# Performance work log

Measured on AMD Instinct MI355X. Metric: run time of the kernel, lower is better.

Reference implementation:

```python
import jax, jax.numpy as jnp
import numpy as np

HEADS = 8
DIM_HEAD = 32
DIM = 256
HIDDEN = HEADS * DIM_HEAD  # 256


def setup_inputs() -> dict:
    key = jax.random.key(0)
    ks = jax.random.split(key, 6)
    B, T, C, H, W = 4, 16, DIM, 32, 32
    x = jax.random.normal(ks[0], (B, T, C, H, W), dtype=jnp.float32)
    rel_pos = jax.random.normal(ks[1], (HEADS, T, T), dtype=jnp.float32)
    # 1x1 conv weights == channel-mixing matrices
    w_qkv = jax.random.normal(ks[2], (3 * HIDDEN, C), dtype=jnp.float32) * (C ** -0.5)
    b_qkv = jnp.zeros((3 * HIDDEN,), dtype=jnp.float32)
    w_out = jax.random.normal(ks[3], (C, HIDDEN), dtype=jnp.float32) * (HIDDEN ** -0.5)
    b_out = jnp.zeros((C,), dtype=jnp.float32)
    return {"x": x, "rel_pos": rel_pos, "w_qkv": w_qkv, "b_qkv": b_qkv,
            "w_out": w_out, "b_out": b_out}


def reference(x, rel_pos, w_qkv, b_qkv, w_out, b_out):
    B, T, C, H, W = x.shape
    scale = DIM_HEAD ** -0.5
    # 1x1 conv QKV projection: (B,T,C,H,W) x (3*hidden, C) -> (B,T,H,W,3*hidden)
    qkv = jnp.einsum('btchw,oc->bthwo', x, w_qkv) + b_qkv
    q, k, v = jnp.split(qkv, 3, axis=-1)
    # split heads: (B,T,H,W,heads,dim_head); attention over T per (b,h,w,head)
    q = q.reshape(B, T, H, W, HEADS, DIM_HEAD) * scale
    k = k.reshape(B, T, H, W, HEADS, DIM_HEAD)
    v = v.reshape(B, T, H, W, HEADS, DIM_HEAD)
    # sim: (B,H,W,heads,T,T)
    sim = jnp.einsum('bihwnd,bjhwnd->bhwnij', q, k)
    sim = sim + rel_pos  # (heads,T,T) broadcasts over (B,H,W)
    attn = jax.nn.softmax(sim, axis=-1)
    out = jnp.einsum('bhwnij,bjhwnd->bihwnd', attn, v)  # (B,T,H,W,heads,dh)
    out = out.reshape(B, T, H, W, HIDDEN)
    # 1x1 conv output projection back to C channels
    y = jnp.einsum('bthwe,ce->bthwc', out, w_out) + b_out
    return jnp.transpose(y, (0, 1, 4, 2, 3))  # (B,T,C,H,W)
```

## Files before the change

### kernel.cpp

```cpp
#include <hip/hip_runtime.h>
#include <hip/hip_bf16.h>

typedef __attribute__((ext_vector_type(8))) short bf16x8;
typedef __attribute__((ext_vector_type(4))) float f32x4;
typedef __attribute__((ext_vector_type(16))) float f32x16;

namespace {

constexpr int kT = 16;
constexpr int kC = 256;
constexpr int kHW = 1024;

__device__ __forceinline__ unsigned short f2bf(float f) {
  unsigned int x;
  __builtin_memcpy(&x, &f, 4);
  x += 0x7fff + ((x >> 16) & 1);
  return (unsigned short)(x >> 16);
}
__device__ __forceinline__ unsigned int pack2(float a, float b) {
  return (unsigned int)f2bf(a) | ((unsigned int)f2bf(b) << 16);
}

__global__ __launch_bounds__(256) void prep(const float* __restrict__ x,
                                            const float* __restrict__ wqkv,
                                            const float* __restrict__ wout,
                                            unsigned short* __restrict__ xT,
                                            unsigned short* __restrict__ wAll) {
  __shared__ unsigned short ts[64 * 72];
  const int bx = blockIdx.x;
  const int tid = threadIdx.x;
  if (bx < 4096) {
    const int cc = bx & 3, hc = (bx >> 2) & 15, t = (bx >> 6) & 15, b = bx >> 10;
    const int c0 = cc * 64, hw0 = hc * 64;
    {
      const int ci = tid >> 2, j = tid & 3;
      const float* xrow = x + (((size_t)(b * 16 + t) * 256 + c0 + ci) * 1024) + hw0;
#pragma unroll
      for (int u = 0; u < 4; ++u) {
        const int chunk = j + u * 4;
        const float4 v = *(const float4*)(xrow + chunk * 4);
        const int hwl = chunk * 4;
        ts[(hwl + 0) * 72 + ci] = f2bf(v.x);
        ts[(hwl + 1) * 72 + ci] = f2bf(v.y);
        ts[(hwl + 2) * 72 + ci] = f2bf(v.z);
        ts[(hwl + 3) * 72 + ci] = f2bf(v.w);
      }
    }
    __syncthreads();
    {
      const int hwp = tid >> 2, jp = tid & 3;
      const uint4 a = *(const uint4*)&ts[hwp * 72 + jp * 16];
      const uint4 bq = *(const uint4*)&ts[hwp * 72 + jp * 16 + 8];
      unsigned short* dst =
          xT + ((size_t)((b * 1024 + hw0 + hwp) * 16 + t) * 256) + c0 + jp * 16;
      *(uint4*)dst = a;
      *(uint4*)(dst + 8) = bq;
    }
  } else {
    const int g = bx - 4096;
    const int row_l = tid >> 3;
    const int seg = tid & 7;
    const float* src;
    int srow;
    if (g < 24) { src = wqkv; srow = (g % 3) * 256 + (g / 3) * 32 + row_l; }
    else        { src = wout; srow = (g - 24) * 32 + row_l; }
    const float* s = src + (size_t)srow * 256 + seg * 32;
    unsigned short* d = wAll + ((size_t)(g * 32 + row_l)) * 256 + seg * 32;
#pragma unroll
    for (int u = 0; u < 8; ++u) {
      const float4 v = *(const float4*)(s + u * 4);
      uint2 p;
      p.x = pack2(v.x, v.y);
      p.y = pack2(v.z, v.w);
      *(uint2*)(d + u * 4) = p;
    }
  }
}

constexpr int kWBStride = 264;
constexpr int kWBTile = 32 * kWBStride;
constexpr int kWB = 2 * kWBTile;
constexpr int kSite = 1824;
constexpr int kSmem = kWB + 8 * kSite;
static_assert(kSmem * 2 <= 65536, "LDS budget");

__global__ __launch_bounds__(512, 2) void attn_main(
    const unsigned short* __restrict__ xT,
    const float* __restrict__ rel,
    const unsigned short* __restrict__ wAll,
    const float* __restrict__ bqkv,
    const float* __restrict__ bout,
    float* __restrict__ out) {
  __shared__ __align__(16) unsigned short smem[kSmem];
  const int tid = threadIdx.x;
  const int lane = tid & 63;
  const int wave = tid >> 6;
  const int quad = lane >> 4;
  const int lrow = lane & 15;
  const int half = lane >> 5;
  const int n32 = lane & 31;
  const int b = blockIdx.x >> 6;
  const int hw0 = (blockIdx.x & 63) * 16;
  const int site0 = hw0 + wave * 2;

  bf16x8 ax[16];
  {
    const unsigned short* xs =
        xT + (((size_t)(b * 1024 + site0 + (n32 >> 4))) << 12) + lrow * 256;
#pragma unroll
    for (int ks = 0; ks < 16; ++ks)
      ax[ks] = *(const bf16x8*)(xs + ks * 16 + half * 8);
  }

  unsigned short* qb = smem + kWB + wave * kSite;
  unsigned short* kb = qb + 640;
  unsigned short* vt = qb + 1280;

  const int stageDst = (tid >> 4) * kWBStride + (tid & 15) * 16;
  const int stageSrcOff = (tid >> 4) * 256 + (tid & 15) * 16;

  uint4 pr0, pr1;
  {
    const unsigned short* sp = wAll + stageSrcOff;
    pr0 = *(const uint4*)sp;
    pr1 = *(const uint4*)(sp + 8);
  }

  const f32x4 zero4 = {0.f, 0.f, 0.f, 0.f};
  const float scale = 0.17677669529663687f;
  bf16x8 ao[2][8];

  auto qkv_tile = [&](int g, float bias) -> f32x16 {
    __syncthreads();
    unsigned short* WBc = smem + (g & 1) * kWBTile;
    *(uint4*)(WBc + stageDst) = pr0;
    *(uint4*)(WBc + stageDst + 8) = pr1;
    {
      const unsigned short* sp = wAll + (size_t)(g + 1) * 32 * 256 + stageSrcOff;
      pr0 = *(const uint4*)sp;
      pr1 = *(const uint4*)(sp + 8);
    }
    __syncthreads();
    f32x16 acc;
#pragma unroll
    for (int i = 0; i < 16; ++i) acc[i] = bias;
    const unsigned short* br = WBc + n32 * kWBStride + half * 8;
#pragma unroll
    for (int ks = 0; ks < 16; ++ks) {
      const bf16x8 bf = *(const bf16x8*)(br + ks * 16);
      acc = __builtin_amdgcn_mfma_f32_32x32x16_bf16(ax[ks], bf, acc, 0, 0, 0);
    }
    return acc;
  };

#pragma unroll 1
  for (int h = 0; h < 8; ++h) {
    const f32x16 qacc = qkv_tile(h * 3 + 0, bqkv[h * 32 + n32]);
    const f32x16 kacc = qkv_tile(h * 3 + 1, bqkv[256 + h * 32 + n32]);
    const f32x16 vacc = qkv_tile(h * 3 + 2, bqkv[512 + h * 32 + n32]);
    float rl[4];
#pragma unroll
    for (int r = 0; r < 4; ++r) rl[r] = rel[h * 256 + (quad * 4 + r) * 16 + lrow];

#pragma unroll
    for (int s = 0; s < 2; ++s) {
#pragma unroll
      for (int rr = 0; rr < 8; ++rr) {
        const int t = (rr & 3) + 8 * (rr >> 2) + 4 * half;
        qb[t * 40 + n32] = f2bf(qacc[8 * s + rr]);
        kb[t * 40 + n32] = f2bf(kacc[8 * s + rr]);
      }
#pragma unroll
      for (int rp = 0; rp < 4; ++rp) {
        const int rr = rp * 2;
        const int t = (rr & 3) + 8 * (rr >> 2) + 4 * half;
        *(unsigned int*)&vt[n32 * 16 + t] =
            pack2(vacc[8 * s + rr], vacc[8 * s + rr + 1]);
      }
      const bf16x8 qf = *(const bf16x8*)(qb + lrow * 40 + quad * 8);
      const bf16x8 kf = *(const bf16x8*)(kb + lrow * 40 + quad * 8);
      const f32x4 sim = __builtin_amdgcn_mfma_f32_16x16x32_bf16(qf, kf, zero4, 0, 0, 0);
      float p[4], inv[4];
#pragma unroll
      for (int r = 0; r < 4; ++r) {
        const float v = sim[r] * scale + rl[r];
        float m = v;
        for (int off = 8; off; off >>= 1) m = fmaxf(m, __shfl_xor(m, off));
        const float e = __expf(v - m);
        float sum = e;
        for (int off = 8; off; off >>= 1) sum += __shfl_xor(sum, off);
        p[r] = e;
        inv[r] = 1.0f / sum;
      }
      unsigned short* pb = kb;
#pragma unroll
      for (int r = 0; r < 4; ++r) pb[(quad * 4 + r) * 24 + lrow] = f2bf(p[r]);
      bf16x8 pf, vf0, vf1;
      if (quad < 2) {
        pf = *(const bf16x8*)(pb + lrow * 24 + quad * 8);
        vf0 = *(const bf16x8*)(vt + lrow * 16 + quad * 8);
        vf1 = *(const bf16x8*)(vt + (16 + lrow) * 16 + quad * 8);
      } else {
#pragma unroll
        for (int j = 0; j < 8; ++j) { pf[j] = 0; vf0[j] = 0; vf1[j] = 0; }
      }
      const f32x4 o0 = __builtin_amdgcn_mfma_f32_16x16x32_bf16(pf, vf0, zero4, 0, 0, 0);
      const f32x4 o1 = __builtin_amdgcn_mfma_f32_16x16x32_bf16(pf, vf1, zero4, 0, 0, 0);
#pragma unroll
      for (int r = 0; r < 4; ++r) {
        const int t = quad * 4 + r;
        qb[t * 40 + lrow] = f2bf(o0[r] * inv[r]);
        qb[t * 40 + 16 + lrow] = f2bf(o1[r] * inv[r]);
      }
      ao[s][h] = *(const bf16x8*)(qb + lrow * 40 + quad * 8);
    }
  }

  __syncthreads();
  float* fbuf = (float*)smem;
  float* ob = out + ((size_t)b << 22);
#pragma unroll 1
  for (int cc = 0; cc < 8; ++cc) {
#pragma unroll
    for (int sub = 0; sub < 2; ++sub) {
      const int c = cc * 32 + sub * 16 + lrow;
      const float bias = bout[c];
      f32x4 y0 = {bias, bias, bias, bias};
      f32x4 y1 = {bias, bias, bias, bias};
#pragma unroll
      for (int ks = 0; ks < 8; ++ks) {
        const bf16x8 wf =
            *(const bf16x8*)(wAll + (size_t)(768 + c) * 256 + ks * 32 + quad * 8);
        y0 = __builtin_amdgcn_mfma_f32_16x16x32_bf16(ao[0][ks], wf, y0, 0, 0, 0);
        y1 = __builtin_amdgcn_mfma_f32_16x16x32_bf16(ao[1][ks], wf, y1, 0, 0, 0);
      }
#pragma unroll
      for (int r = 0; r < 4; ++r) {
        const int t = quad * 4 + r;
        const int L = (t * 32 + sub * 16 + lrow) * 17 + wave * 2;
        fbuf[L] = y0[r];
        fbuf[L + 1] = y1[r];
      }
    }
    __syncthreads();
    {
      const int t = tid >> 5, cl = tid & 31;
      float v[16];
#pragma unroll
      for (int i = 0; i < 16; ++i) v[i] = fbuf[tid * 17 + i];
      float* dst = ob + ((size_t)(t * 256 + cc * 32 + cl)) * 1024 + hw0;
#pragma unroll
      for (int u = 0; u < 4; ++u) {
        float4 q;
        q.x = v[u * 4]; q.y = v[u * 4 + 1]; q.z = v[u * 4 + 2]; q.w = v[u * 4 + 3];
        *(float4*)(dst + u * 4) = q;
      }
    }
    __syncthreads();
  }
}

constexpr int kHWT = 4;
constexpr int kXsTStride = kC * kHWT + 8;
constexpr int kXSize = kT * kXsTStride;
constexpr int kWsOff = kXSize;
constexpr int kWsStride = 264;
constexpr int kWsSize = 32 * kWsStride;
constexpr int kQbOff = kWsOff + kWsSize;
constexpr int kQbWave = 1792;
constexpr int kLdsElems = kQbOff + 4 * kQbWave;

__global__ __launch_bounds__(256, 2) void fused_temporal_attn(
    const float* __restrict__ x, const float* __restrict__ rel,
    const float* __restrict__ wqkv, const float* __restrict__ bqkv,
    const float* __restrict__ wout, const float* __restrict__ bout,
    float* __restrict__ out) {
  __shared__ __align__(16) unsigned short smem[kLdsElems];
  const int tid = threadIdx.x;
  const int lane = tid & 63;
  const int wave = tid >> 6;
  const int quad = lane >> 4;
  const int lrow = lane & 15;
  const int b = blockIdx.x >> 8;
  const int tile = blockIdx.x & 255;
  const int hw0 = tile * kHWT;
  {
    const float* xb = x + (size_t)b * kT * kC * kHW + hw0;
#pragma unroll
    for (int it = 0; it < 16; ++it) {
      int idx = it * 256 + tid;
      int t = idx >> 8, c = idx & 255;
      const float4 v = *(const float4*)(xb + (size_t)(t * kC + c) * kHW);
      uint2 p;
      p.x = pack2(v.x, v.y);
      p.y = pack2(v.z, v.w);
      *(uint2*)&smem[t * kXsTStride + c * kHWT] = p;
    }
  }
  __syncthreads();
  bf16x8 ax[8];
#pragma unroll
  for (int ks = 0; ks < 8; ++ks) {
    bf16x8 f;
#pragma unroll
    for (int j = 0; j < 8; ++j) {
      int c = ks * 32 + quad * 8 + j;
      f[j] = (short)smem[lrow * kXsTStride + c * kHWT + wave];
    }
    ax[ks] = f;
  }
  unsigned short* qb = &smem[kQbOff + wave * kQbWave];
  unsigned short* kbuf = qb + 512;
  unsigned short* vtb = qb + 1024;
  unsigned short* pb = qb + 1536;
  const f32x4 zero4 = {0.f, 0.f, 0.f, 0.f};
  bf16x8 ao[8];
  for (int head = 0; head < 8; ++head) {
    for (int sel = 0; sel < 3; ++sel) {
      __syncthreads();
      {
        const float* wbp = wqkv + (size_t)(sel * 256 + head * 32) * kC;
#pragma unroll
        for (int i = 0; i < 8; ++i) {
          int seg = i * 256 + tid;
          int d = seg >> 6, s = seg & 63;
          const float4 v = *(const float4*)(wbp + d * kC + s * 4);
          uint2 p;
          p.x = pack2(v.x, v.y);
          p.y = pack2(v.z, v.w);
          *(uint2*)&smem[kWsOff + d * kWsStride + s * 4] = p;
        }
      }
      __syncthreads();
      float bias0 = bqkv[sel * 256 + head * 32 + lrow];
      float bias1 = bqkv[sel * 256 + head * 32 + 16 + lrow];
      f32x4 acc0 = {bias0, bias0, bias0, bias0};
      f32x4 acc1 = {bias1, bias1, bias1, bias1};
#pragma unroll
      for (int ks = 0; ks < 8; ++ks) {
        bf16x8 b0 = *(const bf16x8*)&smem[kWsOff + lrow * kWsStride + ks * 32 + quad * 8];
        bf16x8 b1 = *(const bf16x8*)&smem[kWsOff + (16 + lrow) * kWsStride + ks * 32 + quad * 8];
        acc0 = __builtin_amdgcn_mfma_f32_16x16x32_bf16(ax[ks], b0, acc0, 0, 0, 0);
        acc1 = __builtin_amdgcn_mfma_f32_16x16x32_bf16(ax[ks], b1, acc1, 0, 0, 0);
      }
      if (sel < 2) {
        unsigned short* dst = sel ? kbuf : qb;
#pragma unroll
        for (int r = 0; r < 4; ++r) {
          int row = quad * 4 + r;
          dst[row * 32 + lrow] = f2bf(acc0[r]);
          dst[row * 32 + 16 + lrow] = f2bf(acc1[r]);
        }
      } else {
#pragma unroll
        for (int r = 0; r < 4; ++r) {
          int row = quad * 4 + r;
          vtb[lrow * 16 + row] = f2bf(acc0[r]);
          vtb[(16 + lrow) * 16 + row] = f2bf(acc1[r]);
        }
      }
    }
    bf16x8 qf = *(const bf16x8*)&qb[lrow * 32 + quad * 8];
    bf16x8 kf = *(const bf16x8*)&kbuf[lrow * 32 + quad * 8];
    f32x4 sim = __builtin_amdgcn_mfma_f32_16x16x32_bf16(qf, kf, zero4, 0, 0, 0);
    const float scale = 0.17677669529663687f;
    float p[4], rsum[4];
#pragma unroll
    for (int r = 0; r < 4; ++r) {
      int i = quad * 4 + r;
      float v = sim[r] * scale + rel[head * 256 + i * 16 + lrow];
      float m = v;
      for (int off = 8; off; off >>= 1) m = fmaxf(m, __shfl_xor(m, off));
      float e = __expf(v - m);
      float s = e;
      for (int off = 8; off; off >>= 1) s += __shfl_xor(s, off);
      p[r] = e;
      rsum[r] = s;
    }
#pragma unroll
    for (int r = 0; r < 4; ++r) pb[(quad * 4 + r) * 16 + lrow] = f2bf(p[r]);
    bf16x8 pf, vf0, vf1;
    if (quad < 2) {
      pf = *(const bf16x8*)&pb[lrow * 16 + quad * 8];
      vf0 = *(const bf16x8*)&vtb[lrow * 16 + quad * 8];
      vf1 = *(const bf16x8*)&vtb[(16 + lrow) * 16 + quad * 8];
    } else {
#pragma unroll
      for (int j = 0; j < 8; ++j) { pf[j] = 0; vf0[j] = 0; vf1[j] = 0; }
    }
    f32x4 o0 = __builtin_amdgcn_mfma_f32_16x16x32_bf16(pf, vf0, zero4, 0, 0, 0);
    f32x4 o1 = __builtin_amdgcn_mfma_f32_16x16x32_bf16(pf, vf1, zero4, 0, 0, 0);
#pragma unroll
    for (int r = 0; r < 4; ++r) {
      int t = quad * 4 + r;
      float inv = 1.0f / rsum[r];
      qb[t * 32 + lrow] = f2bf(o0[r] * inv);
      qb[t * 32 + 16 + lrow] = f2bf(o1[r] * inv);
    }
    ao[head] = *(const bf16x8*)&qb[lrow * 32 + quad * 8];
  }
  float* ob = out + (size_t)b * kT * kC * kHW + hw0 + wave;
#pragma unroll 1
  for (int nt = 0; nt < 16; ++nt) {
    int c = nt * 16 + lrow;
    float bias = bout[c];
    f32x4 y = {bias, bias, bias, bias};
#pragma unroll
    for (int ks = 0; ks < 8; ++ks) {
      const float4 w0 = *(const float4*)(wout + (size_t)c * kC + ks * 32 + quad * 8);
      const float4 w1 = *(const float4*)(wout + (size_t)c * kC + ks * 32 + quad * 8 + 4);
      bf16x8 wf;
      wf[0] = (short)f2bf(w0.x); wf[1] = (short)f2bf(w0.y);
      wf[2] = (short)f2bf(w0.z); wf[3] = (short)f2bf(w0.w);
      wf[4] = (short)f2bf(w1.x); wf[5] = (short)f2bf(w1.y);
      wf[6] = (short)f2bf(w1.z); wf[7] = (short)f2bf(w1.w);
      y = __builtin_amdgcn_mfma_f32_16x16x32_bf16(ao[ks], wf, y, 0, 0, 0);
    }
#pragma unroll
    for (int r = 0; r < 4; ++r) {
      int t = quad * 4 + r;
      ob[(size_t)(t * kC + c) * kHW] = y[r];
    }
  }
}

}

extern "C" void kernel_launch(void* const* d_in, const int* in_sizes, int n_in,
                              void* d_out, int out_size, void* d_ws, size_t ws_size,
                              hipStream_t stream) {
  const float* x = (const float*)d_in[0];
  const float* rel = (const float*)d_in[1];
  const float* wqkv = (const float*)d_in[2];
  const float* bqkv = (const float*)d_in[3];
  const float* wout = (const float*)d_in[4];
  const float* bout = (const float*)d_in[5];
  float* out = (float*)d_out;
  (void)in_sizes; (void)n_in; (void)out_size;

  constexpr size_t kXTElems = (size_t)4 * 1024 * 16 * 256;
  constexpr size_t kWAllElems = 1024 * 256;
  constexpr size_t kNeed = (kXTElems + kWAllElems) * sizeof(unsigned short);

  if (ws_size >= kNeed) {
    unsigned short* xT = (unsigned short*)d_ws;
    unsigned short* wAll = xT + kXTElems;
    prep<<<4096 + 32, 256, 0, stream>>>(x, wqkv, wout, xT, wAll);
    attn_main<<<256, 512, 0, stream>>>(xT, rel, wAll, bqkv, bout, out);
  } else {
    fused_temporal_attn<<<1024, 256, 0, stream>>>(x, rel, wqkv, bqkv, wout, bout, out);
  }
}
```

Baseline: 243.9 us.

## Stage QKV weights via direct global-to-LDS loads with XOR swizzle and smaller blocks

Pre-swizzles the QKV weight tiles in the prep kernel so attn_main can copy them straight into LDS with global_load_lds, replacing the register-staged copies and padded strides. Blocks shrink to 256 threads covering 8 sites each, launched as 512 blocks with a remapped block order, and the head loop is fully unrolled with ping-pong buffers and fewer barriers. The output-store transpose is reworked to match the smaller block. The goal is less register pressure and staging overhead plus better occupancy and overlap. The cost is that each weight tile is now loaded by twice as many blocks.

```diff
diff --git a/kernel.cpp b/kernel.cpp
--- a/kernel.cpp
+++ b/kernel.cpp
@@ -65,33 +65,37 @@
     if (g < 24) { src = wqkv; srow = (g % 3) * 256 + (g / 3) * 32 + row_l; }
     else        { src = wout; srow = (g - 24) * 32 + row_l; }
     const float* s = src + (size_t)srow * 256 + seg * 32;
-    unsigned short* d = wAll + ((size_t)(g * 32 + row_l)) * 256 + seg * 32;
 #pragma unroll
     for (int u = 0; u < 8; ++u) {
       const float4 v = *(const float4*)(s + u * 4);
       uint2 p;
       p.x = pack2(v.x, v.y);
       p.y = pack2(v.z, v.w);
-      *(uint2*)(d + u * 4) = p;
-    }
-  }
-}
-
-constexpr int kWBStride = 264;
-constexpr int kWBTile = 32 * kWBStride;
-constexpr int kWB = 2 * kWBTile;
+      unsigned short* d;
+      if (g < 24) {
+        int byte = row_l * 512 + (seg * 32 + u * 4) * 2;
+        byte ^= (row_l & 7) << 4;
+        d = wAll + ((size_t)g << 13) + (byte >> 1);
+      } else {
+        d = wAll + ((size_t)(g * 32 + row_l)) * 256 + seg * 32 + u * 4;
+      }
+      *(uint2*)d = p;
+    }
+  }
+}
+
 constexpr int kSite = 1824;
-constexpr int kSmem = kWB + 8 * kSite;
-static_assert(kSmem * 2 <= 65536, "LDS budget");
-
-__global__ __launch_bounds__(512, 2) void attn_main(
+
+__global__ __launch_bounds__(256, 2) void attn_main(
     const unsigned short* __restrict__ xT,
     const float* __restrict__ rel,
     const unsigned short* __restrict__ wAll,
     const float* __restrict__ bqkv,
     const float* __restrict__ bout,
     float* __restrict__ out) {
-  __shared__ __align__(16) unsigned short smem[kSmem];
+  __shared__ __align__(16) unsigned short WB0[32 * 256];
+  __shared__ __align__(16) unsigned short WB1[32 * 256];
+  __shared__ __align__(16) unsigned short SREST[9216];
   const int tid = threadIdx.x;
   const int lane = tid & 63;
   const int wave = tid >> 6;
@@ -99,8 +103,10 @@
   const int lrow = lane & 15;
   const int half = lane >> 5;
   const int n32 = lane & 31;
-  const int b = blockIdx.x >> 6;
-  const int hw0 = (blockIdx.x & 63) * 16;
+  const int bid = blockIdx.x;
+  const int vid = (bid & 7) * 64 + (bid >> 3);
+  const int b = vid >> 7;
+  const int hw0 = (vid & 127) * 8;
   const int site0 = hw0 + wave * 2;
 
   bf16x8 ax[16];
@@ -112,52 +118,55 @@
       ax[ks] = *(const bf16x8*)(xs + ks * 16 + half * 8);
   }
 
-  unsigned short* qb = smem + kWB + wave * kSite;
+  unsigned short* qb = SREST + wave * kSite;
   unsigned short* kb = qb + 640;
   unsigned short* vt = qb + 1280;
 
-  const int stageDst = (tid >> 4) * kWBStride + (tid & 15) * 16;
-  const int stageSrcOff = (tid >> 4) * 256 + (tid & 15) * 16;
-
-  uint4 pr0, pr1;
-  {
-    const unsigned short* sp = wAll + stageSrcOff;
-    pr0 = *(const uint4*)sp;
-    pr1 = *(const uint4*)(sp + 8);
-  }
+  auto stage = [&](unsigned short* dst, int g) {
+    const unsigned short* src =
+        wAll + ((size_t)g << 13) + (wave * 4) * 512 + lane * 8;
+#pragma unroll
+    for (int i = 0; i < 4; ++i) {
+      __builtin_amdgcn_global_load_lds(
+          (const __attribute__((address_space(1))) void*)(src + i * 512),
+          (__attribute__((address_space(3))) void*)(dst + (wave * 4 + i) * 512),
+          16, 0, 0);
+    }
+  };
+
+  auto mfma_tile = [&](const unsigned short* WBc, float bias) -> f32x16 {
+    f32x16 acc;
+#pragma unroll
+    for (int i = 0; i < 16; ++i) acc[i] = bias;
+    const int rswz = (n32 & 7) << 4;
+    const int b0 = n32 * 512 + half * 16;
+    const char* base = (const char*)WBc;
+#pragma unroll
+    for (int ks = 0; ks < 16; ++ks) {
+      const bf16x8 bf = *(const bf16x8*)(base + ((b0 + ks * 32) ^ rswz));
+      acc = __builtin_amdgcn_mfma_f32_32x32x16_bf16(ax[ks], bf, acc, 0, 0, 0);
+    }
+    return acc;
+  };
 
   const f32x4 zero4 = {0.f, 0.f, 0.f, 0.f};
   const float scale = 0.17677669529663687f;
   bf16x8 ao[2][8];
 
-  auto qkv_tile = [&](int g, float bias) -> f32x16 {
-    __syncthreads();
-    unsigned short* WBc = smem + (g & 1) * kWBTile;
-    *(uint4*)(WBc + stageDst) = pr0;
-    *(uint4*)(WBc + stageDst + 8) = pr1;
-    {
-      const unsigned short* sp = wAll + (size_t)(g + 1) * 32 * 256 + stageSrcOff;
-      pr0 = *(const uint4*)sp;
-      pr1 = *(const uint4*)(sp + 8);
-    }
-    __syncthreads();
-    f32x16 acc;
-#pragma unroll
-    for (int i = 0; i < 16; ++i) acc[i] = bias;
-    const unsigned short* br = WBc + n32 * kWBStride + half * 8;
-#pragma unroll
-    for (int ks = 0; ks < 16; ++ks) {
-      const bf16x8 bf = *(const bf16x8*)(br + ks * 16);
-      acc = __builtin_amdgcn_mfma_f32_32x32x16_bf16(ax[ks], bf, acc, 0, 0, 0);
-    }
-    return acc;
-  };
-
-#pragma unroll 1
-  for (int h = 0; h < 8; ++h) {
-    const f32x16 qacc = qkv_tile(h * 3 + 0, bqkv[h * 32 + n32]);
-    const f32x16 kacc = qkv_tile(h * 3 + 1, bqkv[256 + h * 32 + n32]);
-    const f32x16 vacc = qkv_tile(h * 3 + 2, bqkv[512 + h * 32 + n32]);
+  stage(WB0, 0);
+  __syncthreads();
+
+  auto head_body = [&](int h, unsigned short* WA, unsigned short* WBx) {
+    const int g = h * 3;
+    stage(WBx, g + 1);
+    const f32x16 qacc = mfma_tile(WA, bqkv[h * 32 + n32]);
+    __syncthreads();
+    stage(WA, g + 2);
+    const f32x16 kacc = mfma_tile(WBx, bqkv[256 + h * 32 + n32]);
+    __syncthreads();
+    stage(WBx, g + 3);
+    const f32x16 vacc = mfma_tile(WA, bqkv[512 + h * 32 + n32]);
+
     float rl[4];
 #pragma unroll
     for (int r = 0; r < 4; ++r) rl[r] = rel[h * 256 + (quad * 4 + r) * 16 + lrow];
@@ -214,10 +223,20 @@
       }
       ao[s][h] = *(const bf16x8*)(qb + lrow * 40 + quad * 8);
     }
-  }
+    __syncthreads();
+  };
+
+  head_body(0, WB0, WB1);
+  head_body(1, WB1, WB0);
+  head_body(2, WB0, WB1);
+  head_body(3, WB1, WB0);
+  head_body(4, WB0, WB1);
+  head_body(5, WB1, WB0);
+  head_body(6, WB0, WB1);
+  head_body(7, WB1, WB0);
 
   __syncthreads();
-  float* fbuf = (float*)smem;
+  float* FB = (float*)SREST;
   float* ob = out + ((size_t)b << 22);
 #pragma unroll 1
   for (int cc = 0; cc < 8; ++cc) {
@@ -236,25 +255,25 @@
       }
 #pragma unroll
       for (int r = 0; r < 4; ++r) {
-        const int t = quad * 4 + r;
-        const int L = (t * 32 + sub * 16 + lrow) * 17 + wave * 2;
-        fbuf[L] = y0[r];
-        fbuf[L + 1] = y1[r];
-      }
-    }
-    __syncthreads();
-    {
-      const int t = tid >> 5, cl = tid & 31;
-      float v[16];
-#pragma unroll
-      for (int i = 0; i < 16; ++i) v[i] = fbuf[tid * 17 + i];
+        const int L = ((quad * 4 + r) * 32 + sub * 16 + lrow) * 9 + wave * 2;
+        FB[L] = y0[r];
+        FB[L + 1] = y1[r];
+      }
+    }
+    __syncthreads();
+#pragma unroll
+    for (int q2 = 0; q2 < 2; ++q2) {
+      const int L = tid + q2 * 256;
+      const int t = L >> 5, cl = L & 31;
+      float v[8];
+#pragma unroll
+      for (int i = 0; i < 8; ++i) v[i] = FB[L * 9 + i];
       float* dst = ob + ((size_t)(t * 256 + cc * 32 + cl)) * 1024 + hw0;
-#pragma unroll
-      for (int u = 0; u < 4; ++u) {
-        float4 q;
-        q.x = v[u * 4]; q.y = v[u * 4 + 1]; q.z = v[u * 4 + 2]; q.w = v[u * 4 + 3];
-        *(float4*)(dst + u * 4) = q;
-      }
+      float4 st0, st1;
+      st0.x = v[0]; st0.y = v[1]; st0.z = v[2]; st0.w = v[3];
+      st1.x = v[4]; st1.y = v[5]; st1.z = v[6]; st1.w = v[7];
+      *(float4*)dst = st0;
+      *(float4*)(dst + 4) = st1;
     }
     __syncthreads();
   }
@@ -446,7 +465,7 @@
     unsigned short* xT = (unsigned short*)d_ws;
     unsigned short* wAll = xT + kXTElems;
     prep<<<4096 + 32, 256, 0, stream>>>(x, wqkv, wout, xT, wAll);
-    attn_main<<<256, 512, 0, stream>>>(xT, rel, wAll, bqkv, bout, out);
+    attn_main<<<512, 256, 0, stream>>>(xT, rel, wAll, bqkv, bout, out);
   } else {
     fused_temporal_attn<<<1024, 256, 0, stream>>>(x, rel, wqkv, bqkv, wout, bout, out);
   }
```

Result: faster. 220.4 us (-9.6%).
